# Performance work log

Hardware: AMD Instinct MI355X
Metric: run time of the kernel (lower is better)

Reference implementation:

```python
import jax, jax.numpy as jnp
import numpy as np

B, S_DEC, S_ENC, D, H = 2, 2048, 2048, 1024, 16
HD = D // H  # 64


def setup_inputs() -> dict:
    key = jax.random.key(0)
    ks = jax.random.split(key, 12)
    s = 0.02
    return {
        "dec_hidden_state": jax.random.normal(ks[0], (B, S_DEC, D), jnp.float32),
        "enc_hidden_state": jax.random.normal(ks[1], (B, S_ENC, D), jnp.float32),
        "mask": jnp.ones((B, S_ENC, S_DEC), jnp.int32),
        "Wq": jax.random.normal(ks[2], (H, D, HD), jnp.float32) * s,
        "bq": jax.random.normal(ks[3], (H, HD), jnp.float32) * s,
        "Wk": jax.random.normal(ks[4], (H, D, HD), jnp.float32) * s,
        "bk": jax.random.normal(ks[5], (H, HD), jnp.float32) * s,
        "Wv": jax.random.normal(ks[6], (H, D, HD), jnp.float32) * s,
        "bv": jax.random.normal(ks[7], (H, HD), jnp.float32) * s,
        "Wo": jax.random.normal(ks[8], (D, D), jnp.float32) * s,
        "bo": jax.random.normal(ks[9], (D,), jnp.float32) * s,
    }


def reference(dec_hidden_state, enc_hidden_state, mask, Wq, bq, Wk, bk, Wv, bv, Wo, bo):
    # NOTE: original module swaps args: query <- enc_hidden_state, key/value <- dec_hidden_state.
    # q: [B,H,S_enc,HD], k/v: [B,H,S_dec,HD]
    q = jnp.einsum("bqd,hdk->bhqk", enc_hidden_state, Wq) + bq[None, :, None, :]
    k = jnp.einsum("bsd,hdk->bhsk", dec_hidden_state, Wk) + bk[None, :, None, :]
    v = jnp.einsum("bsd,hdk->bhsk", dec_hidden_state, Wv) + bv[None, :, None, :]
    scores = jnp.einsum("bhqk,bhsk->bhqs", q, k) / jnp.sqrt(jnp.asarray(HD, q.dtype))
    scores = jnp.where(mask[:, None, :, :] == 0, jnp.asarray(-jnp.inf, scores.dtype), scores)
    weights = jax.nn.softmax(scores, axis=-1)
    attn = jnp.einsum("bhqs,bhsk->bhqk", weights, v)  # [B,H,S_enc,HD]
    # concat heads along last dim (same order as torch.cat over head list)
    attn = jnp.transpose(attn, (0, 2, 1, 3)).reshape(B, S_ENC, D)
    return attn @ Wo + bo
```

## Files before the change

### kernel.cpp

```cpp
#include <hip/hip_runtime.h>
#include <math.h>
#include <stdint.h>


typedef unsigned short ushort_t;
typedef __attribute__((ext_vector_type(8))) short short8;
typedef __attribute__((ext_vector_type(4))) float floatx4;

__device__ __forceinline__ ushort_t f2bf(float x){
  unsigned u = __float_as_uint(x);
  u += 0x7fffu + ((u >> 16) & 1u);
  return (ushort_t)(u >> 16);
}
__device__ __forceinline__ unsigned pk2bf(float a, float b){
#if __has_builtin(__builtin_amdgcn_cvt_pk_bf16_f32)
  typedef __attribute__((ext_vector_type(2))) __bf16 bf2_t;
  bf2_t r = __builtin_amdgcn_cvt_pk_bf16_f32(a, b);
  return *(unsigned*)&r;
#else
  return (unsigned)f2bf(a) | ((unsigned)f2bf(b) << 16);
#endif
}
__device__ __forceinline__ floatx4 mfma16(short8 a, short8 b, floatx4 c){
  return __builtin_amdgcn_mfma_f32_16x16x32_bf16(a, b, c, 0, 0, 0);
}
__device__ __forceinline__ void gload16(const void* g, void* l){
  __builtin_amdgcn_global_load_lds((const __attribute__((address_space(1))) void*)g,
                                   (__attribute__((address_space(3))) void*)l, 16, 0, 0);
}

__global__ __launch_bounds__(256)
void prep_kernel(const float* __restrict__ enc, const float* __restrict__ dec,
                 const float* __restrict__ Wq, const float* __restrict__ Wk,
                 const float* __restrict__ Wv, const float* __restrict__ Wo,
                 const int* __restrict__ mask,
                 ushort_t* __restrict__ encb, ushort_t* __restrict__ decb,
                 ushort_t* __restrict__ WqT, ushort_t* __restrict__ WkT,
                 ushort_t* __restrict__ WvT, ushort_t* __restrict__ WoT,
                 unsigned long long* __restrict__ mb)
{
  __shared__ float t[64][65];
  const int bx = blockIdx.x, tid = threadIdx.x;
  if (bx < 8192){
    const float* src = (bx < 4096) ? enc : dec;
    ushort_t*    dst = (bx < 4096) ? encb : decb;
    int i = ((bx & 4095) * 256 + tid) * 4;
    const float4 v = *(const float4*)(src + i);
    unsigned long long p = (unsigned long long)pk2bf(v.x, v.y)
                         | ((unsigned long long)pk2bf(v.z, v.w) << 32);
    *(unsigned long long*)(dst + i) = p;
  } else if (bx < 8960){
    const int id = bx - 8192;
    const int zz = id >> 4, yy = id & 15;
    const int which = zz >> 4, head = zz & 15;
    const float* src = (which == 0) ? Wq : (which == 1) ? Wk : Wv;
    ushort_t*    dst = (which == 0) ? WqT : (which == 1) ? WkT : WvT;
    const long sb = (long)head * 65536;
    const int r0 = yy * 64;
    #pragma unroll
    for (int i = 0; i < 4; i++){
      int idx = i*256 + tid;
      int r = idx >> 4, c4 = idx & 15;
      const float4 v = *(const float4*)&src[sb + (long)(r0 + r)*64 + c4*4];
      t[r][c4*4+0] = v.x; t[r][c4*4+1] = v.y;
      t[r][c4*4+2] = v.z; t[r][c4*4+3] = v.w;
    }
    __syncthreads();
    #pragma unroll
    for (int i = 0; i < 4; i++){
      int idx = i*256 + tid;
      int cr = idx >> 4, rq = idx & 15;
      unsigned long long p =
          (unsigned long long)pk2bf(t[rq*4+0][cr], t[rq*4+1][cr])
        | ((unsigned long long)pk2bf(t[rq*4+2][cr], t[rq*4+3][cr]) << 32);
      *(unsigned long long*)&dst[sb + (long)cr*1024 + r0 + rq*4] = p;
    }
  } else if (bx < 9216){
    const int id = bx - 8960;
    const int r0 = (id >> 4) * 64, c0 = (id & 15) * 64;
    #pragma unroll
    for (int i = 0; i < 4; i++){
      int idx = i*256 + tid;
      int r = idx >> 4, c4 = idx & 15;
      const float4 v = *(const float4*)&Wo[(long)(r0 + r)*1024 + c0 + c4*4];
      t[r][c4*4+0] = v.x; t[r][c4*4+1] = v.y;
      t[r][c4*4+2] = v.z; t[r][c4*4+3] = v.w;
    }
    __syncthreads();
    #pragma unroll
    for (int i = 0; i < 4; i++){
      int idx = i*256 + tid;
      int cr = idx >> 4, rq = idx & 15;
      unsigned long long p =
          (unsigned long long)pk2bf(t[rq*4+0][cr], t[rq*4+1][cr])
        | ((unsigned long long)pk2bf(t[rq*4+2][cr], t[rq*4+3][cr]) << 32);
      *(unsigned long long*)&WoT[(long)(c0 + cr)*1024 + r0 + rq*4] = p;
    }
  } else {
    long gid = (long)(bx - 9216) * 256 + tid;
    unsigned long long bal = __ballot(mask[gid] != 0);
    if ((tid & 63) == 0) mb[gid >> 6] = bal;
  }
}

__global__ __launch_bounds__(256, 3)
void gemm_qkv_kernel(const ushort_t* __restrict__ encb, const ushort_t* __restrict__ decb,
                     const ushort_t* __restrict__ WqT, const ushort_t* __restrict__ WkT,
                     const ushort_t* __restrict__ WvT,
                     const float* __restrict__ bq, const float* __restrict__ bk,
                     const float* __restrict__ bv,
                     ushort_t* __restrict__ Qb, ushort_t* __restrict__ Kbf,
                     ushort_t* __restrict__ Vtb)
{
  __shared__ ushort_t At[2*4096];
  __shared__ ushort_t Bt[2*4096];
  const int tid = threadIdx.x;
  const int wave = tid >> 6, lane = tid & 63;
  const int quad = lane >> 4, l16 = lane & 15;
  const int z = blockIdx.z;
  const ushort_t *A, *BT; const float* bias; ushort_t* outp;
  int m0, n0; long outAdj = 0;
  float qs = 1.0f;
  if (z == 0){ A = encb; BT = WqT; bias = bq; outp = Qb;  m0 = blockIdx.x*128; n0 = blockIdx.y*128;
               qs = 0.18033688011112042f; }
  else if (z == 1){ A = decb; BT = WkT; bias = bk; outp = Kbf; m0 = blockIdx.x*128; n0 = blockIdx.y*128; }
  else {
    int id = blockIdx.x*8 + blockIdx.y;
    int vb = id >> 7, rem = id & 127;
    m0 = ((rem >> 4) & 7) * 128; n0 = (rem & 15) * 128;
    A = WvT; BT = decb + (long)vb*2097152; bias = bv; outp = Vtb; outAdj = (long)vb*2097152;
  }
  const int K = 1024;

  const int c0 = tid, c1 = 256 + tid;
  const ushort_t* gA0 = A  + (long)(m0 + (c0 >> 2))*K + (c0 & 3)*8;
  const ushort_t* gA1 = A  + (long)(m0 + (c1 >> 2))*K + (c1 & 3)*8;
  const ushort_t* gB0 = BT + (long)(n0 + (c0 >> 2))*K + (c0 & 3)*8;
  const ushort_t* gB1 = BT + (long)(n0 + (c1 >> 2))*K + (c1 & 3)*8;

  floatx4 acc[4][4];
  #pragma unroll
  for (int mt = 0; mt < 4; mt++)
    #pragma unroll
    for (int nt = 0; nt < 4; nt++)
      acc[mt][nt] = (floatx4){0.f, 0.f, 0.f, 0.f};

  {
    char* Ad = (char*)At + wave*1024;
    char* Bd = (char*)Bt + wave*1024;
    gload16(gA0, Ad); gload16(gA1, Ad + 4096);
    gload16(gB0, Bd); gload16(gB1, Bd + 4096);
    gA0 += 32; gA1 += 32; gB0 += 32; gB1 += 32;
  }

  const int moff = (wave & 1) * 64, noff = (wave >> 1) * 64;
  int cur = 0;
  for (int k0 = 0; k0 < K; k0 += 32){
    asm volatile("s_waitcnt vmcnt(0)" ::: "memory");
    __builtin_amdgcn_sched_barrier(0);
    __builtin_amdgcn_s_barrier();
    __builtin_amdgcn_sched_barrier(0);
    if (k0 + 32 < K){
      char* An = (char*)At + (cur^1)*8192 + wave*1024;
      char* Bn = (char*)Bt + (cur^1)*8192 + wave*1024;
      gload16(gA0, An); gload16(gA1, An + 4096);
      gload16(gB0, Bn); gload16(gB1, Bn + 4096);
      gA0 += 32; gA1 += 32; gB0 += 32; gB1 += 32;
    }
    short8 af[4], bfr[4];
    #pragma unroll
    for (int t = 0; t < 4; t++){
      af[t]  = *(const short8*)&At[cur*4096 + (moff + t*16 + l16)*32 + quad*8];
      bfr[t] = *(const short8*)&Bt[cur*4096 + (noff + t*16 + l16)*32 + quad*8];
    }
    #pragma unroll
    for (int mt = 0; mt < 4; mt++)
      #pragma unroll
      for (int nt = 0; nt < 4; nt++)
        acc[mt][nt] = mfma16(bfr[nt], af[mt], acc[mt][nt]);
    asm volatile("s_waitcnt lgkmcnt(0)" ::: "memory");
    __builtin_amdgcn_sched_barrier(0);
    __builtin_amdgcn_s_barrier();
    __builtin_amdgcn_sched_barrier(0);
    cur ^= 1;
  }

  #pragma unroll
  for (int mt = 0; mt < 4; mt++){
    #pragma unroll
    for (int nt = 0; nt < 4; nt++){
      floatx4 v = acc[mt][nt];
      if (z < 2){
        const int s   = m0 + moff + mt*16 + l16;
        const int ch0 = n0 + noff + nt*16 + quad*4;
        const float4 b4 = *(const float4*)&bias[ch0];
        uint2 pk;
        pk.x = pk2bf((v[0] + b4.x)*qs, (v[1] + b4.y)*qs);
        pk.y = pk2bf((v[2] + b4.z)*qs, (v[3] + b4.w)*qs);
        *(unsigned long long*)&outp[(long)s*1024 + ch0] = *(unsigned long long*)&pk;
      } else {
        const int ch = m0 + moff + mt*16 + l16;
        const int s0 = n0 + noff + nt*16 + quad*4;
        const float bb = bias[ch];
        uint2 pk;
        pk.x = pk2bf(v[0] + bb, v[1] + bb);
        pk.y = pk2bf(v[2] + bb, v[3] + bb);
        *(unsigned long long*)&outp[outAdj + (long)ch*2048 + s0] = *(unsigned long long*)&pk;
      }
    }
  }
}

__global__ __launch_bounds__(256, 2)
void gemm_o_kernel(const ushort_t* __restrict__ A, const ushort_t* __restrict__ BT,
                   const float* __restrict__ bias, float* __restrict__ outf)
{
  __shared__ ushort_t At[2*4096];
  __shared__ ushort_t Bt[2*2048];
  const int tid = threadIdx.x;
  const int wave = tid >> 6, lane = tid & 63;
  const int quad = lane >> 4, l16 = lane & 15;
  const int m0 = blockIdx.x * 128, n0 = blockIdx.y * 64;
  const int K = 1024;

  const int c0 = tid, c1 = 256 + tid;
  const ushort_t* gA0 = A  + (long)(m0 + (c0 >> 2))*K + (c0 & 3)*8;
  const ushort_t* gA1 = A  + (long)(m0 + (c1 >> 2))*K + (c1 & 3)*8;
  const ushort_t* gB0 = BT + (long)(n0 + (c0 >> 2))*K + (c0 & 3)*8;

  floatx4 acc[4][2];
  #pragma unroll
  for (int mt = 0; mt < 4; mt++)
    #pragma unroll
    for (int nt = 0; nt < 2; nt++)
      acc[mt][nt] = (floatx4){0.f, 0.f, 0.f, 0.f};

  {
    char* Ad = (char*)At + wave*1024;
    char* Bd = (char*)Bt + wave*1024;
    gload16(gA0, Ad); gload16(gA1, Ad + 4096);
    gload16(gB0, Bd);
    gA0 += 32; gA1 += 32; gB0 += 32;
  }

  const int moff = (wave & 1) * 64, noff = (wave >> 1) * 32;
  int cur = 0;
  for (int k0 = 0; k0 < K; k0 += 32){
    asm volatile("s_waitcnt vmcnt(0)" ::: "memory");
    __builtin_amdgcn_sched_barrier(0);
    __builtin_amdgcn_s_barrier();
    __builtin_amdgcn_sched_barrier(0);
    if (k0 + 32 < K){
      char* An = (char*)At + (cur^1)*8192 + wave*1024;
      char* Bn = (char*)Bt + (cur^1)*4096 + wave*1024;
      gload16(gA0, An); gload16(gA1, An + 4096);
      gload16(gB0, Bn);
      gA0 += 32; gA1 += 32; gB0 += 32;
    }
    short8 af[4], bfr[2];
    #pragma unroll
    for (int t = 0; t < 4; t++)
      af[t]  = *(const short8*)&At[cur*4096 + (moff + t*16 + l16)*32 + quad*8];
    #pragma unroll
    for (int t = 0; t < 2; t++)
      bfr[t] = *(const short8*)&Bt[cur*2048 + (noff + t*16 + l16)*32 + quad*8];
    #pragma unroll
    for (int mt = 0; mt < 4; mt++)
      #pragma unroll
      for (int nt = 0; nt < 2; nt++)
        acc[mt][nt] = mfma16(bfr[nt], af[mt], acc[mt][nt]);
    asm volatile("s_waitcnt lgkmcnt(0)" ::: "memory");
    __builtin_amdgcn_sched_barrier(0);
    __builtin_amdgcn_s_barrier();
    __builtin_amdgcn_sched_barrier(0);
    cur ^= 1;
  }

  #pragma unroll
  for (int mt = 0; mt < 4; mt++){
    #pragma unroll
    for (int nt = 0; nt < 2; nt++){
      const int s   = m0 + moff + mt*16 + l16;
      const int ch0 = n0 + noff + nt*16 + quad*4;
      const float4 b4 = *(const float4*)&bias[ch0];
      float4 o;
      o.x = acc[mt][nt][0] + b4.x;
      o.y = acc[mt][nt][1] + b4.y;
      o.z = acc[mt][nt][2] + b4.z;
      o.w = acc[mt][nt][3] + b4.w;
      *(float4*)&outf[(long)s*1024 + ch0] = o;
    }
  }
}

#define SM_PB(zA_, zB_, wv_, lsum_, pb_)                              \
  {                                                                   \
    float p0 = __builtin_amdgcn_exp2f((zA_)[0]);                      \
    float p1 = __builtin_amdgcn_exp2f((zA_)[1]);                      \
    float p2 = __builtin_amdgcn_exp2f((zA_)[2]);                      \
    float p3 = __builtin_amdgcn_exp2f((zA_)[3]);                      \
    float p4 = __builtin_amdgcn_exp2f((zB_)[0]);                      \
    float p5 = __builtin_amdgcn_exp2f((zB_)[1]);                      \
    float p6 = __builtin_amdgcn_exp2f((zB_)[2]);                      \
    float p7 = __builtin_amdgcn_exp2f((zB_)[3]);                      \
    if (__builtin_expect(!uni, 0)){                                   \
      const int sh_ = quad*8;                                         \
      p0 = (((wv_) >> (sh_+0)) & 1u) ? p0 : 0.f;                      \
      p1 = (((wv_) >> (sh_+1)) & 1u) ? p1 : 0.f;                      \
      p2 = (((wv_) >> (sh_+2)) & 1u) ? p2 : 0.f;                      \
      p3 = (((wv_) >> (sh_+3)) & 1u) ? p3 : 0.f;                      \
      p4 = (((wv_) >> (sh_+4)) & 1u) ? p4 : 0.f;                      \
      p5 = (((wv_) >> (sh_+5)) & 1u) ? p5 : 0.f;                      \
      p6 = (((wv_) >> (sh_+6)) & 1u) ? p6 : 0.f;                      \
      p7 = (((wv_) >> (sh_+7)) & 1u) ? p7 : 0.f;                      \
    }                                                                 \
    lsum_ += ((p0 + p1) + (p2 + p3)) + ((p4 + p5) + (p6 + p7));       \
    unsigned pk0_ = pk2bf(p0, p1);                                    \
    unsigned pk1_ = pk2bf(p2, p3);                                    \
    unsigned pk2_ = pk2bf(p4, p5);                                    \
    unsigned pk3_ = pk2bf(p6, p7);                                    \
    unsigned tmp_[4] = {pk0_, pk1_, pk2_, pk3_};                      \
    __builtin_memcpy(&(pb_), tmp_, 16);                               \
  }

__global__ __launch_bounds__(512, 4)
void flash_attn_kernel(const ushort_t* __restrict__ Qp, const ushort_t* __restrict__ Kp,
                       const ushort_t* __restrict__ Vt, const unsigned* __restrict__ mb,
                       ushort_t* __restrict__ aout)
{
  __shared__ __align__(16) unsigned char smem_raw[65536];
  ushort_t* KBs = (ushort_t*)smem_raw;
  ushort_t* VBs = KBs + 16384;
  float* mO = (float*)smem_raw;
  float* mL = (float*)(smem_raw + 32768);

  const int tid = threadIdx.x, wave = tid >> 6, lane = tid & 63;
  const int quad = lane >> 4, l16 = lane & 15;
  const int shalf = wave >> 2, w = wave & 3;
  const int bh = blockIdx.x, qt = blockIdx.y;
  const int b = bh >> 4, h = bh & 15;

  const ushort_t* VB = Vt + (long)bh*131072;
  const int q0 = qt*128 + w*32;

  const int l8 = lane >> 3, cl = lane & 7;
  const int r0 = w*16 + l8;
  const int sr0 = (r0 & 35) | ((r0 & 4) << 1) | ((r0 & 16) >> 2);
  const int cg = cl ^ l8;
  const ushort_t* kp0 = Kp + ((long)b*2048 + shalf*1024 + sr0)*1024 + h*64 + cg*8;
  const ushort_t* kp1 = kp0 + 16384;
  const ushort_t* vp0 = VB + (long)r0*2048 + shalf*1024 + cg*8;
  const ushort_t* vp1 = vp0 + 16384;
  const int kdo = shalf*16384 + w*2048;
  const int vdo = 32768 + shalf*16384 + w*2048;

  {
    char* kd = (char*)smem_raw + kdo;
    gload16(kp0, kd); gload16(kp1, kd + 1024);
    char* vd = (char*)smem_raw + vdo;
    gload16(vp0, vd); gload16(vp1, vd + 1024);
    kp0 += 65536; kp1 += 65536; vp0 += 64; vp1 += 64;
  }

  short8 qfA0, qfA1, qfB0, qfB1;
  {
    const long qrowA = ((long)b*2048 + q0 + l16)*1024 + h*64;
    qfA0 = *(const short8*)&Qp[qrowA +      quad*8];
    qfA1 = *(const short8*)&Qp[qrowA + 32 + quad*8];
    const long qrowB = qrowA + 16*1024;
    qfB0 = *(const short8*)&Qp[qrowB +      quad*8];
    qfB1 = *(const short8*)&Qp[qrowB + 32 + quad*8];
  }

  floatx4 accA[4], accB[4];
  #pragma unroll
  for (int ht = 0; ht < 4; ht++){
    accA[ht] = (floatx4){0.f,0.f,0.f,0.f};
    accB[ht] = (floatx4){0.f,0.f,0.f,0.f};
  }
  float lsA = 0.f, lsB = 0.f;

  const uint2* mb2 = (const uint2*)mb;
  const long mbase = (long)b*2048 + q0;
  const int sw8 = l16 & 7;
  const int kc0 = (quad ^ sw8) * 8;
  const int kc1 = kc0 ^ 32;

  int cur = 0;
  for (int st = 0; st < 16; st++){
    const uint2 mwA = mb2[(mbase +      l16)*32 + shalf*16 + st];
    const uint2 mwB = mb2[(mbase + 16 + l16)*32 + shalf*16 + st];
    __builtin_amdgcn_sched_barrier(0);
    if (st < 15){
      char* kd = (char*)smem_raw + kdo + (cur^1)*8192;
      gload16(kp0, kd); gload16(kp1, kd + 1024);
      char* vd = (char*)smem_raw + vdo + (cur^1)*8192;
      gload16(vp0, vd); gload16(vp1, vd + 1024);
      kp0 += 65536; kp1 += 65536; vp0 += 64; vp1 += 64;
      asm volatile("s_waitcnt vmcnt(6)" ::: "memory");
    } else {
      asm volatile("s_waitcnt vmcnt(0)" ::: "memory");
    }
    __builtin_amdgcn_s_barrier();
    __builtin_amdgcn_sched_barrier(0);

    const ushort_t* Kt = KBs + shalf*8192 + cur*4096;
    const ushort_t* Vp = VBs + shalf*8192 + cur*4096;
    const bool uni = __all((mwA.x & mwA.y & mwB.x & mwB.y) == 0xFFFFFFFFu);

    #pragma unroll
    for (int c = 0; c < 2; c++){
      const int rA = (c*2    )*16 + l16;
      const int rB = (c*2 + 1)*16 + l16;
      short8 kA0 = *(const short8*)&Kt[rA*64 + kc0];
      short8 kA1 = *(const short8*)&Kt[rA*64 + kc1];
      short8 kB0 = *(const short8*)&Kt[rB*64 + kc0];
      short8 kB1 = *(const short8*)&Kt[rB*64 + kc1];

      floatx4 zA = (floatx4){0.f,0.f,0.f,0.f};
      zA = mfma16(kA0, qfA0, zA);
      zA = mfma16(kA1, qfA1, zA);
      floatx4 zB = (floatx4){0.f,0.f,0.f,0.f};
      zB = mfma16(kB0, qfA0, zB);
      zB = mfma16(kB1, qfA1, zB);
      const unsigned wvA = c ? mwA.y : mwA.x;
      short8 pbA;
      SM_PB(zA, zB, wvA, lsA, pbA);

      zA = (floatx4){0.f,0.f,0.f,0.f};
      zA = mfma16(kA0, qfB0, zA);
      zA = mfma16(kA1, qfB1, zA);
      zB = (floatx4){0.f,0.f,0.f,0.f};
      zB = mfma16(kB0, qfB0, zB);
      zB = mfma16(kB1, qfB1, zB);
      const unsigned wvB = c ? mwB.y : mwB.x;
      short8 pbB;
      SM_PB(zA, zB, wvB, lsB, pbB);

      const int vcs = ((c*4 + quad) ^ sw8) * 8;
      #pragma unroll
      for (int ht = 0; ht < 4; ht++){
        const short8 vf = *(const short8*)&Vp[(ht*16 + l16)*64 + vcs];
        accA[ht] = mfma16(vf, pbA, accA[ht]);
        accB[ht] = mfma16(vf, pbB, accB[ht]);
      }
    }

    asm volatile("s_waitcnt lgkmcnt(0)" ::: "memory");
    __builtin_amdgcn_sched_barrier(0);
    __builtin_amdgcn_s_barrier();
    __builtin_amdgcn_sched_barrier(0);
    cur ^= 1;
  }

  lsA += __shfl_xor(lsA, 16);
  lsA += __shfl_xor(lsA, 32);
  lsB += __shfl_xor(lsB, 16);
  lsB += __shfl_xor(lsB, 32);

  __syncthreads();
  if (shalf == 1){
    #pragma unroll
    for (int ht = 0; ht < 4; ht++){
      *(floatx4*)&mO[((((w*2 + 0)*4 + ht)*64) + lane)*4] = accA[ht];
      *(floatx4*)&mO[((((w*2 + 1)*4 + ht)*64) + lane)*4] = accB[ht];
    }
    mL[(w*2 + 0)*64 + lane] = lsA;
    mL[(w*2 + 1)*64 + lane] = lsB;
  }
  __syncthreads();
  if (shalf == 0){
    const float invA = 1.0f / (lsA + mL[(w*2 + 0)*64 + lane]);
    const float invB = 1.0f / (lsB + mL[(w*2 + 1)*64 + lane]);
    const long rowoA = ((long)b*2048 + q0 + l16)*1024 + h*64;
    const long rowoB = rowoA + 16*1024;
    #pragma unroll
    for (int ht = 0; ht < 4; ht++){
      const floatx4 oA = *(const floatx4*)&mO[((((w*2 + 0)*4 + ht)*64) + lane)*4];
      uint2 pkA;
      pkA.x = pk2bf((accA[ht][0] + oA[0])*invA, (accA[ht][1] + oA[1])*invA);
      pkA.y = pk2bf((accA[ht][2] + oA[2])*invA, (accA[ht][3] + oA[3])*invA);
      *(unsigned long long*)&aout[rowoA + ht*16 + quad*4] = *(unsigned long long*)&pkA;
      const floatx4 oB = *(const floatx4*)&mO[((((w*2 + 1)*4 + ht)*64) + lane)*4];
      uint2 pkB;
      pkB.x = pk2bf((accB[ht][0] + oB[0])*invB, (accB[ht][1] + oB[1])*invB);
      pkB.y = pk2bf((accB[ht][2] + oB[2])*invB, (accB[ht][3] + oB[3])*invB);
      *(unsigned long long*)&aout[rowoB + ht*16 + quad*4] = *(unsigned long long*)&pkB;
    }
  }
}

extern "C" void kernel_launch(void* const* d_in, const int* in_sizes, int n_in,
                              void* d_out, int out_size, void* d_ws, size_t ws_size,
                              hipStream_t stream) {
  const float* dec  = (const float*)d_in[0];
  const float* enc  = (const float*)d_in[1];
  const int*   mask = (const int*)d_in[2];
  const float* Wq   = (const float*)d_in[3];
  const float* bq   = (const float*)d_in[4];
  const float* Wk   = (const float*)d_in[5];
  const float* bk   = (const float*)d_in[6];
  const float* Wv   = (const float*)d_in[7];
  const float* bv   = (const float*)d_in[8];
  const float* Wo   = (const float*)d_in[9];
  const float* bo   = (const float*)d_in[10];
  float* out = (float*)d_out;

  ushort_t* ws   = (ushort_t*)d_ws;
  ushort_t* encb = ws;
  ushort_t* decb = encb + 4194304;
  ushort_t* Qb   = decb + 4194304;
  ushort_t* Kbf  = Qb   + 4194304;
  ushort_t* Vtb  = Kbf  + 4194304;
  ushort_t* WqT  = Vtb  + 4194304;
  ushort_t* WkT  = WqT  + 1048576;
  ushort_t* WvT  = WkT  + 1048576;
  ushort_t* WoT  = WvT  + 1048576;
  unsigned* Mb   = (unsigned*)(WoT + 1048576);

  prep_kernel<<<41984, 256, 0, stream>>>(enc, dec, Wq, Wk, Wv, Wo, mask,
                                         encb, decb, WqT, WkT, WvT, WoT,
                                         (unsigned long long*)Mb);
  gemm_qkv_kernel<<<dim3(32,8,3), 256, 0, stream>>>(encb, decb, WqT, WkT, WvT,
                                                    bq, bk, bv, Qb, Kbf, Vtb);
  flash_attn_kernel<<<dim3(32,16,1), 512, 0, stream>>>(Qb, Kbf, Vtb, Mb, encb);
  gemm_o_kernel<<<dim3(32,16,1), 256, 0, stream>>>(encb, WoT, bo, out);
}
```

Measured before the change: 244.8 us.

## Move mask bitpacking and Wo transpose into QKV GEMM launch as extra blocks

The mask ballot-packing and the Wo transpose/bf16 conversion move out of the prep kernel and into a fourth z-slice of the QKV GEMM grid. That slice uses grid-stride loops over 224 blocks for the mask and 32 blocks that each transpose 8 tiles. The intent is to shrink the memory-bound prep kernel and hide this side work under the compute-bound GEMM. The cost is that these blocks compete with GEMM blocks for CUs and bandwidth, and the shared memory is now a single aliased buffer.

```diff
diff --git a/kernel.cpp b/kernel.cpp
--- a/kernel.cpp
+++ b/kernel.cpp
@@ -32,12 +32,10 @@
 __global__ __launch_bounds__(256)
 void prep_kernel(const float* __restrict__ enc, const float* __restrict__ dec,
                  const float* __restrict__ Wq, const float* __restrict__ Wk,
-                 const float* __restrict__ Wv, const float* __restrict__ Wo,
-                 const int* __restrict__ mask,
+                 const float* __restrict__ Wv,
                  ushort_t* __restrict__ encb, ushort_t* __restrict__ decb,
                  ushort_t* __restrict__ WqT, ushort_t* __restrict__ WkT,
-                 ushort_t* __restrict__ WvT, ushort_t* __restrict__ WoT,
-                 unsigned long long* __restrict__ mb)
+                 ushort_t* __restrict__ WvT)
 {
   __shared__ float t[64][65];
   const int bx = blockIdx.x, tid = threadIdx.x;
@@ -49,7 +47,7 @@
     unsigned long long p = (unsigned long long)pk2bf(v.x, v.y)
                          | ((unsigned long long)pk2bf(v.z, v.w) << 32);
     *(unsigned long long*)(dst + i) = p;
-  } else if (bx < 8960){
+  } else {
     const int id = bx - 8192;
     const int zz = id >> 4, yy = id & 15;
     const int which = zz >> 4, head = zz & 15;
@@ -75,31 +73,6 @@
         | ((unsigned long long)pk2bf(t[rq*4+2][cr], t[rq*4+3][cr]) << 32);
       *(unsigned long long*)&dst[sb + (long)cr*1024 + r0 + rq*4] = p;
     }
-  } else if (bx < 9216){
-    const int id = bx - 8960;
-    const int r0 = (id >> 4) * 64, c0 = (id & 15) * 64;
-    #pragma unroll
-    for (int i = 0; i < 4; i++){
-      int idx = i*256 + tid;
-      int r = idx >> 4, c4 = idx & 15;
-      const float4 v = *(const float4*)&Wo[(long)(r0 + r)*1024 + c0 + c4*4];
-      t[r][c4*4+0] = v.x; t[r][c4*4+1] = v.y;
-      t[r][c4*4+2] = v.z; t[r][c4*4+3] = v.w;
-    }
-    __syncthreads();
-    #pragma unroll
-    for (int i = 0; i < 4; i++){
-      int idx = i*256 + tid;
-      int cr = idx >> 4, rq = idx & 15;
-      unsigned long long p =
-          (unsigned long long)pk2bf(t[rq*4+0][cr], t[rq*4+1][cr])
-        | ((unsigned long long)pk2bf(t[rq*4+2][cr], t[rq*4+3][cr]) << 32);
-      *(unsigned long long*)&WoT[(long)(c0 + cr)*1024 + r0 + rq*4] = p;
-    }
-  } else {
-    long gid = (long)(bx - 9216) * 256 + tid;
-    unsigned long long bal = __ballot(mask[gid] != 0);
-    if ((tid & 63) == 0) mb[gid >> 6] = bal;
   }
 }
 
@@ -110,14 +83,55 @@
                      const float* __restrict__ bq, const float* __restrict__ bk,
                      const float* __restrict__ bv,
                      ushort_t* __restrict__ Qb, ushort_t* __restrict__ Kbf,
-                     ushort_t* __restrict__ Vtb)
+                     ushort_t* __restrict__ Vtb,
+                     const int* __restrict__ mask, unsigned long long* __restrict__ mbq,
+                     const float* __restrict__ Wo, ushort_t* __restrict__ WoT)
 {
-  __shared__ ushort_t At[2*4096];
-  __shared__ ushort_t Bt[2*4096];
+  __shared__ __align__(16) unsigned char qsmem[32768];
+  ushort_t* At = (ushort_t*)qsmem;
+  ushort_t* Bt = (ushort_t*)(qsmem + 16384);
   const int tid = threadIdx.x;
+  const int z = blockIdx.z;
+
+  if (z == 3){
+    const int id = blockIdx.x*8 + blockIdx.y;
+    if (id < 224){
+      const long total = 8388608;
+      for (long g = (long)id*256 + tid; g < total; g += 224*256){
+        unsigned long long bal = __ballot(mask[g] != 0);
+        if ((tid & 63) == 0) mbq[g >> 6] = bal;
+      }
+    } else {
+      float (*t)[65] = (float(*)[65])qsmem;
+      for (int j = 0; j < 8; j++){
+        const int tl = (id - 224)*8 + j;
+        const int r0 = (tl >> 4) * 64, c0 = (tl & 15) * 64;
+        #pragma unroll
+        for (int i = 0; i < 4; i++){
+          int idx = i*256 + tid;
+          int r = idx >> 4, c4 = idx & 15;
+          const float4 v = *(const float4*)&Wo[(long)(r0 + r)*1024 + c0 + c4*4];
+          t[r][c4*4+0] = v.x; t[r][c4*4+1] = v.y;
+          t[r][c4*4+2] = v.z; t[r][c4*4+3] = v.w;
+        }
+        __syncthreads();
+        #pragma unroll
+        for (int i = 0; i < 4; i++){
+          int idx = i*256 + tid;
+          int cr = idx >> 4, rq = idx & 15;
+          unsigned long long p =
+              (unsigned long long)pk2bf(t[rq*4+0][cr], t[rq*4+1][cr])
+            | ((unsigned long long)pk2bf(t[rq*4+2][cr], t[rq*4+3][cr]) << 32);
+          *(unsigned long long*)&WoT[(long)(c0 + cr)*1024 + r0 + rq*4] = p;
+        }
+        __syncthreads();
+      }
+    }
+    return;
+  }
+
   const int wave = tid >> 6, lane = tid & 63;
   const int quad = lane >> 4, l16 = lane & 15;
-  const int z = blockIdx.z;
   const ushort_t *A, *BT; const float* bias; ushort_t* outp;
   int m0, n0; long outAdj = 0;
   float qs = 1.0f;
@@ -518,11 +532,12 @@
   ushort_t* WoT  = WvT  + 1048576;
   unsigned* Mb   = (unsigned*)(WoT + 1048576);
 
-  prep_kernel<<<41984, 256, 0, stream>>>(enc, dec, Wq, Wk, Wv, Wo, mask,
-                                         encb, decb, WqT, WkT, WvT, WoT,
-                                         (unsigned long long*)Mb);
-  gemm_qkv_kernel<<<dim3(32,8,3), 256, 0, stream>>>(encb, decb, WqT, WkT, WvT,
-                                                    bq, bk, bv, Qb, Kbf, Vtb);
+  prep_kernel<<<8960, 256, 0, stream>>>(enc, dec, Wq, Wk, Wv,
+                                        encb, decb, WqT, WkT, WvT);
+  gemm_qkv_kernel<<<dim3(32,8,4), 256, 0, stream>>>(encb, decb, WqT, WkT, WvT,
+                                                    bq, bk, bv, Qb, Kbf, Vtb,
+                                                    mask, (unsigned long long*)Mb,
+                                                    Wo, WoT);
   flash_attn_kernel<<<dim3(32,16,1), 512, 0, stream>>>(Qb, Kbf, Vtb, Mb, encb);
   gemm_o_kernel<<<dim3(32,16,1), 256, 0, stream>>>(encb, WoT, bo, out);
 }
```

Result: slower. 287.9 us (+17.6%).
